# Kernel tuning notes

Hardware: AMD Instinct MI355X
Metric: run time of the kernel (lower is better)

Reference implementation:

```python
import jax, jax.numpy as jnp
import numpy as np

N_NODES = 100000
N_EDGES = 20000  # hyperedges
NNZ = 800000
D = 128


def setup_inputs() -> dict:
    key = jax.random.key(0)
    ks = jax.random.split(key, 10)
    X = jax.random.normal(ks[0], (N_NODES, D), dtype=jnp.float32)
    X0 = jax.random.normal(ks[1], (N_NODES, D), dtype=jnp.float32)
    degE = jax.random.uniform(ks[2], (N_EDGES, 1), dtype=jnp.float32)
    degV = jax.random.uniform(ks[3], (N_NODES, 1), dtype=jnp.float32)
    alpha = jax.random.uniform(ks[4], (1,), dtype=jnp.float32)
    beta = jax.random.uniform(ks[5], (1,), dtype=jnp.float32)
    W_w = jax.random.normal(ks[6], (D, D), dtype=jnp.float32) / np.sqrt(D)
    g1_src = jax.random.randint(ks[7], (NNZ,), 0, N_NODES, dtype=jnp.int64 if jax.config.read('jax_enable_x64') else jnp.int32)
    g1_dst = jax.random.randint(ks[8], (NNZ,), 0, N_EDGES)
    g2_src = jax.random.randint(ks[9], (NNZ,), 0, N_EDGES)
    g2_dst = jax.random.randint(jax.random.fold_in(key, 99), (NNZ,), 0, N_NODES)
    return {"X": X, "X0": X0, "degE": degE, "degV": degV, "alpha": alpha,
            "beta": beta, "W_w": W_w, "g1_src": g1_src, "g1_dst": g1_dst,
            "g2_src": g2_src, "g2_dst": g2_dst}


def reference(X, X0, degE, degV, alpha, beta, W_w, g1_src, g1_dst, g2_src, g2_dst):
    n_edges = degE.shape[0]
    n_nodes = degV.shape[0]
    a = alpha[0]
    b = beta[0]
    # copy_u_sum(g1, X): gather node rows, scatter-sum into hyperedges
    Xe = jax.ops.segment_sum(X[g1_src], g1_dst, num_segments=n_edges)  # [E, D]
    Xe = Xe * degE
    # copy_u_sum(g2, Xe): gather hyperedge rows, scatter-sum into nodes
    Xv = jax.ops.segment_sum(Xe[g2_src], g2_dst, num_segments=n_nodes)  # [N, D]
    Xv = Xv * degV
    # GCNII-style initial residual + identity mapping
    Xi = (1.0 - a) * Xv + a * X0
    out = (1.0 - b) * Xi + b * (Xi @ W_w.T)  # Linear(bias=False)
    return out
```

## Files before the change

kernel.cpp:

```cpp
#include <hip/hip_runtime.h>

#define DD 128
#define SCAN_CHUNK 2048
#define PAD1 16
#define PAD2 8

typedef __attribute__((ext_vector_type(8))) short bf16x8;
typedef __attribute__((ext_vector_type(4))) float f32x4;

__device__ __forceinline__ short f2bf(float f) {
    union { float f; unsigned u; } x; x.f = f;
    unsigned r = x.u + 0x7FFF + ((x.u >> 16) & 1);
    return (short)(r >> 16);
}

__global__ __launch_bounds__(256)
void k_hist2(const int* __restrict__ g1d, const int* __restrict__ g2d,
             int* __restrict__ cnt1p, int* __restrict__ cnt2p,
             int* __restrict__ rank1, int* __restrict__ rank2,
             int nnz, int no) {
    int gid = blockIdx.x * 256 + threadIdx.x;
    const int* dst; int* cnt; int* rank; int q; int str;
    if (gid < no) { dst = g1d; cnt = cnt1p; rank = rank1; str = PAD1; q = gid; }
    else {
        q = gid - no;
        if (q >= no) return;
        dst = g2d; cnt = cnt2p; rank = rank2; str = PAD2;
    }
    int i = q << 3;
    if (i + 8 <= nnz) {
        int4 d0 = *(const int4*)(dst + i);
        int4 d1 = *(const int4*)(dst + i + 4);
        int r0 = atomicAdd(&cnt[d0.x * str], 1);
        int r1 = atomicAdd(&cnt[d0.y * str], 1);
        int r2 = atomicAdd(&cnt[d0.z * str], 1);
        int r3 = atomicAdd(&cnt[d0.w * str], 1);
        int r4 = atomicAdd(&cnt[d1.x * str], 1);
        int r5 = atomicAdd(&cnt[d1.y * str], 1);
        int r6 = atomicAdd(&cnt[d1.z * str], 1);
        int r7 = atomicAdd(&cnt[d1.w * str], 1);
        *(int4*)(rank + i)     = make_int4(r0, r1, r2, r3);
        *(int4*)(rank + i + 4) = make_int4(r4, r5, r6, r7);
    } else {
        for (; i < nnz; ++i) rank[i] = atomicAdd(&cnt[dst[i] * str], 1);
    }
}

__global__ __launch_bounds__(256)
void k_scan_blocks2(const int* __restrict__ cnt1, int* __restrict__ off1,
                    const int* __restrict__ cnt2, int* __restrict__ off2,
                    int* __restrict__ bsum, int n1, int n2, int nb1) {
    __shared__ int sh[256];
    const int tid = threadIdx.x;
    const int b = blockIdx.x;
    const int* cnt; int* off; int* bs; int n; int lb; int str;
    if (b < nb1) { cnt = cnt1; off = off1; bs = bsum;      n = n1; lb = b;       str = PAD1; }
    else         { cnt = cnt2; off = off2; bs = bsum + 64; n = n2; lb = b - nb1; str = PAD2; }

    const int base = lb * SCAN_CHUNK + tid * 8;
    int v[8];
    int s = 0;
    #pragma unroll
    for (int j = 0; j < 8; ++j) {
        int idx = base + j;
        v[j] = (idx < n) ? cnt[(size_t)idx * str] : 0;
        s += v[j];
    }
    sh[tid] = s;
    __syncthreads();
    for (int d = 1; d < 256; d <<= 1) {
        int y = (tid >= d) ? sh[tid - d] : 0;
        __syncthreads();
        sh[tid] += y;
        __syncthreads();
    }
    int incl = sh[tid];
    int run = incl - s;
    #pragma unroll
    for (int j = 0; j < 8; ++j) {
        int idx = base + j;
        if (idx < n) off[idx] = run;
        run += v[j];
    }
    if (tid == 255) bs[lb] = incl;
}

__global__ void k_scan_top2(int* __restrict__ bsum, int nb1, int nb2) {
    if (threadIdx.x == 0) {
        int run = 0;
        for (int i = 0; i < nb1; ++i) { int t = bsum[i]; bsum[i] = run; run += t; }
    } else if (threadIdx.x == 1) {
        int run = 0;
        for (int i = 0; i < nb2; ++i) { int t = bsum[64 + i]; bsum[64 + i] = run; run += t; }
    }
}

__global__ __launch_bounds__(256)
void k_scan_add2(int* __restrict__ off1, int* __restrict__ off2,
                 const int* __restrict__ bsum, int n1, int n2, int nnz) {
    int gid = blockIdx.x * 256 + threadIdx.x;
    if (gid < n1) {
        off1[gid] += bsum[gid >> 11];
    } else {
        int g = gid - n1;
        if (g < n2) off2[g] += bsum[64 + (g >> 11)];
    }
    if (gid == 0) { off1[n1] = nnz; off2[n2] = nnz; }
}

__global__ __launch_bounds__(256)
void k_fill2(const int* __restrict__ g1d, const int* __restrict__ g1s,
             const int* __restrict__ off1, const int* __restrict__ rank1,
             int* __restrict__ srcs1,
             const int* __restrict__ g2d, const int* __restrict__ g2s,
             const int* __restrict__ off2, const int* __restrict__ rank2,
             int* __restrict__ srcs2,
             int nnz, int nq) {
    int gid = blockIdx.x * 256 + threadIdx.x;
    const int* dst; const int* src; const int* off; const int* rank; int* out; int q;
    if (gid < nq) { dst = g1d; src = g1s; off = off1; rank = rank1; out = srcs1; q = gid; }
    else {
        q = gid - nq;
        if (q >= nq) return;
        dst = g2d; src = g2s; off = off2; rank = rank2; out = srcs2;
    }
    int i = q << 2;
    if (i + 4 <= nnz) {
        int4 d = *(const int4*)(dst + i);
        int4 s = *(const int4*)(src + i);
        int4 r = *(const int4*)(rank + i);
        int o0 = off[d.x];
        int o1 = off[d.y];
        int o2 = off[d.z];
        int o3 = off[d.w];
        out[o0 + r.x] = s.x;
        out[o1 + r.y] = s.y;
        out[o2 + r.z] = s.z;
        out[o3 + r.w] = s.w;
    } else {
        for (; i < nnz; ++i) out[off[dst[i]] + rank[i]] = src[i];
    }
}

__global__ __launch_bounds__(256)
void k_edge_gather(const float* __restrict__ X, const int* __restrict__ off,
                   const int* __restrict__ srcs, const float* __restrict__ degE,
                   float* __restrict__ Xe, int n_edges) {
    int gid = blockIdx.x * 256 + threadIdx.x;
    int e = gid >> 5;
    if (e >= n_edges) return;
    int k = (gid & 31) << 2;
    int beg = off[e], end = off[e + 1];
    float4 acc0 = {0, 0, 0, 0}, acc1 = {0, 0, 0, 0};
    float4 acc2 = {0, 0, 0, 0}, acc3 = {0, 0, 0, 0};
    int j = beg;
    for (; j + 8 <= end; j += 8) {
        int s0 = srcs[j + 0];
        int s1 = srcs[j + 1];
        int s2 = srcs[j + 2];
        int s3 = srcs[j + 3];
        int s4 = srcs[j + 4];
        int s5 = srcs[j + 5];
        int s6 = srcs[j + 6];
        int s7 = srcs[j + 7];
        float4 v0 = *(const float4*)(X + (size_t)s0 * DD + k);
        float4 v1 = *(const float4*)(X + (size_t)s1 * DD + k);
        float4 v2 = *(const float4*)(X + (size_t)s2 * DD + k);
        float4 v3 = *(const float4*)(X + (size_t)s3 * DD + k);
        float4 v4 = *(const float4*)(X + (size_t)s4 * DD + k);
        float4 v5 = *(const float4*)(X + (size_t)s5 * DD + k);
        float4 v6 = *(const float4*)(X + (size_t)s6 * DD + k);
        float4 v7 = *(const float4*)(X + (size_t)s7 * DD + k);
        acc0.x += v0.x; acc0.y += v0.y; acc0.z += v0.z; acc0.w += v0.w;
        acc1.x += v1.x; acc1.y += v1.y; acc1.z += v1.z; acc1.w += v1.w;
        acc2.x += v2.x; acc2.y += v2.y; acc2.z += v2.z; acc2.w += v2.w;
        acc3.x += v3.x; acc3.y += v3.y; acc3.z += v3.z; acc3.w += v3.w;
        acc0.x += v4.x; acc0.y += v4.y; acc0.z += v4.z; acc0.w += v4.w;
        acc1.x += v5.x; acc1.y += v5.y; acc1.z += v5.z; acc1.w += v5.w;
        acc2.x += v6.x; acc2.y += v6.y; acc2.z += v6.z; acc2.w += v6.w;
        acc3.x += v7.x; acc3.y += v7.y; acc3.z += v7.z; acc3.w += v7.w;
    }
    for (; j < end; ++j) {
        int s = srcs[j];
        float4 v = *(const float4*)(X + (size_t)s * DD + k);
        acc0.x += v.x; acc0.y += v.y; acc0.z += v.z; acc0.w += v.w;
    }
    float f = degE[e];
    float4 o;
    o.x = f * ((acc0.x + acc1.x) + (acc2.x + acc3.x));
    o.y = f * ((acc0.y + acc1.y) + (acc2.y + acc3.y));
    o.z = f * ((acc0.z + acc1.z) + (acc2.z + acc3.z));
    o.w = f * ((acc0.w + acc1.w) + (acc2.w + acc3.w));
    *(float4*)(Xe + (size_t)e * DD + k) = o;
}

__global__ __launch_bounds__(256)
void k_node_gather(const float* __restrict__ Xe, const int* __restrict__ off,
                   const int* __restrict__ srcs, const float* __restrict__ degV,
                   const float* __restrict__ X0, const float* __restrict__ alphaP,
                   float* __restrict__ Xi, int n_nodes) {
    int gid = blockIdx.x * 256 + threadIdx.x;
    int v = gid >> 5;
    if (v >= n_nodes) return;
    int k = (gid & 31) << 2;
    int beg = off[v], end = off[v + 1];
    float4 acc0 = {0, 0, 0, 0}, acc1 = {0, 0, 0, 0};
    int j = beg;
    for (; j + 4 <= end; j += 4) {
        int s0 = srcs[j + 0];
        int s1 = srcs[j + 1];
        int s2 = srcs[j + 2];
        int s3 = srcs[j + 3];
        float4 v0 = *(const float4*)(Xe + (size_t)s0 * DD + k);
        float4 v1 = *(const float4*)(Xe + (size_t)s1 * DD + k);
        float4 v2 = *(const float4*)(Xe + (size_t)s2 * DD + k);
        float4 v3 = *(const float4*)(Xe + (size_t)s3 * DD + k);
        acc0.x += v0.x; acc0.y += v0.y; acc0.z += v0.z; acc0.w += v0.w;
        acc1.x += v1.x; acc1.y += v1.y; acc1.z += v1.z; acc1.w += v1.w;
        acc0.x += v2.x; acc0.y += v2.y; acc0.z += v2.z; acc0.w += v2.w;
        acc1.x += v3.x; acc1.y += v3.y; acc1.z += v3.z; acc1.w += v3.w;
    }
    for (; j < end; ++j) {
        int s = srcs[j];
        float4 x = *(const float4*)(Xe + (size_t)s * DD + k);
        acc0.x += x.x; acc0.y += x.y; acc0.z += x.z; acc0.w += x.w;
    }
    float a = alphaP[0];
    float f = (1.0f - a) * degV[v];
    float4 x0 = *(const float4*)(X0 + (size_t)v * DD + k);
    float4 o;
    o.x = f * (acc0.x + acc1.x) + a * x0.x;
    o.y = f * (acc0.y + acc1.y) + a * x0.y;
    o.z = f * (acc0.z + acc1.z) + a * x0.z;
    o.w = f * (acc0.w + acc1.w) + a * x0.w;
    *(float4*)(Xi + (size_t)v * DD + k) = o;
}

__global__ __launch_bounds__(256)
void k_prep_w(const float* __restrict__ W, const float* __restrict__ betaP,
              short* __restrict__ Mbf) {
    int gid = blockIdx.x * 256 + threadIdx.x;
    if (gid >= DD * DD / 8) return;
    int c  = gid >> 4;
    int k0 = (gid & 15) << 3;
    float b = betaP[0], ib = 1.0f - b;
    const float* p = W + c * DD + k0;
    float4 lo = *(const float4*)p, hi = *(const float4*)(p + 4);
    float v[8] = {lo.x, lo.y, lo.z, lo.w, hi.x, hi.y, hi.z, hi.w};
    bf16x8 t;
    #pragma unroll
    for (int j = 0; j < 8; ++j) {
        float m = b * v[j] + ((k0 + j) == c ? ib : 0.0f);
        t[j] = f2bf(m);
    }
    *(bf16x8*)(Mbf + (size_t)c * DD + k0) = t;
}

__global__ __launch_bounds__(256)
void k_gemm_mfma(float* xio, const short* __restrict__ Mbf, int n_rows) {
    const int lane = threadIdx.x & 63;
    const int wid  = threadIdx.x >> 6;
    const int m16  = lane & 15;
    const int quad = lane >> 4;
    const int kq   = quad * 8;

    const int strip = blockIdx.x * 4 + wid;
    const int row0 = strip * 16;
    if (row0 >= n_rows) return;

    int arow = row0 + m16;
    if (arow >= n_rows) arow = n_rows - 1;
    const float* xr = xio + (size_t)arow * DD;

    bf16x8 af[4];
    #pragma unroll
    for (int kf = 0; kf < 4; ++kf) {
        const float* p = xr + kf * 32 + kq;
        float4 lo = *(const float4*)p;
        float4 hi = *(const float4*)(p + 4);
        bf16x8 t;
        t[0] = f2bf(lo.x); t[1] = f2bf(lo.y); t[2] = f2bf(lo.z); t[3] = f2bf(lo.w);
        t[4] = f2bf(hi.x); t[5] = f2bf(hi.y); t[6] = f2bf(hi.z); t[7] = f2bf(hi.w);
        af[kf] = t;
    }

    #pragma unroll
    for (int nt = 0; nt < 8; ++nt) {
        const short* mr = Mbf + (size_t)(nt * 16 + m16) * DD + kq;
        f32x4 acc = {0.f, 0.f, 0.f, 0.f};
        #pragma unroll
        for (int kf = 0; kf < 4; ++kf) {
            bf16x8 bfrag = *(const bf16x8*)(mr + kf * 32);
            acc = __builtin_amdgcn_mfma_f32_16x16x32_bf16(af[kf], bfrag, acc, 0, 0, 0);
        }
        const int col = nt * 16 + m16;
        #pragma unroll
        for (int r = 0; r < 4; ++r) {
            int row = row0 + quad * 4 + r;
            if (row < n_rows)
                xio[(size_t)row * DD + col] = acc[r];
        }
    }
}

extern "C" void kernel_launch(void* const* d_in, const int* in_sizes, int n_in,
                              void* d_out, int out_size, void* d_ws, size_t ws_size,
                              hipStream_t stream) {
    const float* X     = (const float*)d_in[0];
    const float* X0    = (const float*)d_in[1];
    const float* degE  = (const float*)d_in[2];
    const float* degV  = (const float*)d_in[3];
    const float* alpha = (const float*)d_in[4];
    const float* beta  = (const float*)d_in[5];
    const float* W     = (const float*)d_in[6];
    const int*   g1s   = (const int*)d_in[7];
    const int*   g1d   = (const int*)d_in[8];
    const int*   g2s   = (const int*)d_in[9];
    const int*   g2d   = (const int*)d_in[10];
    float* out = (float*)d_out;

    const int n_nodes = in_sizes[3];
    const int n_edges = in_sizes[2];
    const int nnz     = in_sizes[7];

    int*   wsi   = (int*)d_ws;
    float* Xe    = (float*)d_ws;
    int*   rank1 = wsi;
    int*   rank2 = wsi + nnz;
    size_t o     = (size_t)n_edges * DD;
    int*   off1  = wsi + o;          o += n_edges + 1;
    int*   off2  = wsi + o;          o += n_nodes + 1;
    size_t srcs_base = o;
    int*   srcs1 = wsi + o;          o += nnz;
    int*   srcs2 = wsi + o;          o += nnz;
    int*   bsum  = wsi + o;          o += 128;
    short* Mbf   = (short*)(wsi + o); o += DD * DD / 2;
    int*   cnt1p = wsi + srcs_base;
    int*   cnt2p = cnt1p + (size_t)n_edges * PAD1;

    hipMemsetAsync(cnt1p, 0,
                   ((size_t)n_edges * PAD1 + (size_t)n_nodes * PAD2) * sizeof(int),
                   stream);

    const int nb1 = (n_edges + SCAN_CHUNK - 1) / SCAN_CHUNK;
    const int nb2 = (n_nodes + SCAN_CHUNK - 1) / SCAN_CHUNK;
    const int no  = (nnz + 7) / 8;
    const int oblb = (2 * no + 255) / 256;
    const int nq  = (nnz + 3) / 4;
    const int qblb = (2 * nq + 255) / 256;

    k_prep_w<<<(DD * DD / 8 + 255) / 256, 256, 0, stream>>>(W, beta, Mbf);

    k_hist2<<<oblb, 256, 0, stream>>>(g1d, g2d, cnt1p, cnt2p, rank1, rank2, nnz, no);
    k_scan_blocks2<<<nb1 + nb2, 256, 0, stream>>>(cnt1p, off1, cnt2p, off2, bsum,
                                                  n_edges, n_nodes, nb1);
    k_scan_top2<<<1, 64, 0, stream>>>(bsum, nb1, nb2);
    k_scan_add2<<<(n_edges + n_nodes + 255) / 256, 256, 0, stream>>>(
        off1, off2, bsum, n_edges, n_nodes, nnz);
    k_fill2<<<qblb, 256, 0, stream>>>(g1d, g1s, off1, rank1, srcs1,
                                      g2d, g2s, off2, rank2, srcs2, nnz, nq);

    k_edge_gather<<<(n_edges * 32 + 255) / 256, 256, 0, stream>>>(
        X, off1, srcs1, degE, Xe, n_edges);
    k_node_gather<<<(n_nodes * 32 + 255) / 256, 256, 0, stream>>>(
        Xe, off2, srcs2, degV, X0, alpha, out, n_nodes);

    const int nstrips = (n_nodes + 15) / 16;
    k_gemm_mfma<<<(nstrips + 3) / 4, 256, 0, stream>>>(out, Mbf, n_nodes);
}
```

Before: 407.6 us.

## Use per-XCD histogram counters with workgroup-scope L2 atomics for CSR build

Replaces the padded, device-scope atomic counters in the histogram pass with eight per-XCD counter arrays. Each CU increments the copy for its own XCC using workgroup-scope atomics, which can resolve in that XCD's L2 rather than needing device-wide coherence. The XCC id is packed into the top bits of each rank. The scan sums the per-XCD counts, scan_add produces a per-XCD base offset table, and the fill step uses tag and base to place entries. This trades cheaper atomics for extra counter reads in the scan, a new base table, and a dependence on workgroup-scope atomics staying coherent within one XCD.

After: 412.9 us. Within noise of the previous version (+1.3%).

```diff
diff --git a/kernel.cpp b/kernel.cpp
--- a/kernel.cpp
+++ b/kernel.cpp
@@ -2,8 +2,7 @@
 
 #define DD 128
 #define SCAN_CHUNK 2048
-#define PAD1 16
-#define PAD2 8
+#define NXCD 8
 
 typedef __attribute__((ext_vector_type(8))) short bf16x8;
 typedef __attribute__((ext_vector_type(4))) float f32x4;
@@ -14,48 +13,63 @@
     return (short)(r >> 16);
 }
 
+__device__ __forceinline__ int xcc_id() {
+    int x;
+    asm volatile("s_getreg_b32 %0, hwreg(HW_REG_XCC_ID)" : "=s"(x));
+    return x & (NXCD - 1);
+}
+
+__device__ __forceinline__ int l2_atomic_inc(int* p) {
+    return __hip_atomic_fetch_add(p, 1, __ATOMIC_RELAXED, __HIP_MEMORY_SCOPE_WORKGROUP);
+}
+
 __global__ __launch_bounds__(256)
 void k_hist2(const int* __restrict__ g1d, const int* __restrict__ g2d,
-             int* __restrict__ cnt1p, int* __restrict__ cnt2p,
+             int* __restrict__ cnt1x, int* __restrict__ cnt2x,
              int* __restrict__ rank1, int* __restrict__ rank2,
-             int nnz, int no) {
+             int nnz, int no, int str1, int str2) {
     int gid = blockIdx.x * 256 + threadIdx.x;
     const int* dst; int* cnt; int* rank; int q; int str;
-    if (gid < no) { dst = g1d; cnt = cnt1p; rank = rank1; str = PAD1; q = gid; }
+    if (gid < no) { dst = g1d; cnt = cnt1x; rank = rank1; str = str1; q = gid; }
     else {
         q = gid - no;
         if (q >= no) return;
-        dst = g2d; cnt = cnt2p; rank = rank2; str = PAD2;
-    }
+        dst = g2d; cnt = cnt2x; rank = rank2; str = str2;
+    }
+    const int xc = xcc_id();
+    int* mycnt = cnt + (size_t)xc * str;
+    const int tag = xc << 24;
+
     int i = q << 3;
     if (i + 8 <= nnz) {
         int4 d0 = *(const int4*)(dst + i);
         int4 d1 = *(const int4*)(dst + i + 4);
-        int r0 = atomicAdd(&cnt[d0.x * str], 1);
-        int r1 = atomicAdd(&cnt[d0.y * str], 1);
-        int r2 = atomicAdd(&cnt[d0.z * str], 1);
-        int r3 = atomicAdd(&cnt[d0.w * str], 1);
-        int r4 = atomicAdd(&cnt[d1.x * str], 1);
-        int r5 = atomicAdd(&cnt[d1.y * str], 1);
-        int r6 = atomicAdd(&cnt[d1.z * str], 1);
-        int r7 = atomicAdd(&cnt[d1.w * str], 1);
-        *(int4*)(rank + i)     = make_int4(r0, r1, r2, r3);
-        *(int4*)(rank + i + 4) = make_int4(r4, r5, r6, r7);
+        int r0 = l2_atomic_inc(&mycnt[d0.x]);
+        int r1 = l2_atomic_inc(&mycnt[d0.y]);
+        int r2 = l2_atomic_inc(&mycnt[d0.z]);
+        int r3 = l2_atomic_inc(&mycnt[d0.w]);
+        int r4 = l2_atomic_inc(&mycnt[d1.x]);
+        int r5 = l2_atomic_inc(&mycnt[d1.y]);
+        int r6 = l2_atomic_inc(&mycnt[d1.z]);
+        int r7 = l2_atomic_inc(&mycnt[d1.w]);
+        *(int4*)(rank + i)     = make_int4(tag | r0, tag | r1, tag | r2, tag | r3);
+        *(int4*)(rank + i + 4) = make_int4(tag | r4, tag | r5, tag | r6, tag | r7);
     } else {
-        for (; i < nnz; ++i) rank[i] = atomicAdd(&cnt[dst[i] * str], 1);
+        for (; i < nnz; ++i) rank[i] = tag | l2_atomic_inc(&mycnt[dst[i]]);
     }
 }
 
 __global__ __launch_bounds__(256)
 void k_scan_blocks2(const int* __restrict__ cnt1, int* __restrict__ off1,
                     const int* __restrict__ cnt2, int* __restrict__ off2,
-                    int* __restrict__ bsum, int n1, int n2, int nb1) {
+                    int* __restrict__ bsum, int n1, int n2, int nb1,
+                    int str1, int str2) {
     __shared__ int sh[256];
     const int tid = threadIdx.x;
     const int b = blockIdx.x;
     const int* cnt; int* off; int* bs; int n; int lb; int str;
-    if (b < nb1) { cnt = cnt1; off = off1; bs = bsum;      n = n1; lb = b;       str = PAD1; }
-    else         { cnt = cnt2; off = off2; bs = bsum + 64; n = n2; lb = b - nb1; str = PAD2; }
+    if (b < nb1) { cnt = cnt1; off = off1; bs = bsum;      n = n1; lb = b;       str = str1; }
+    else         { cnt = cnt2; off = off2; bs = bsum + 64; n = n2; lb = b - nb1; str = str2; }
 
     const int base = lb * SCAN_CHUNK + tid * 8;
     int v[8];
@@ -63,8 +77,13 @@
     #pragma unroll
     for (int j = 0; j < 8; ++j) {
         int idx = base + j;
-        v[j] = (idx < n) ? cnt[(size_t)idx * str] : 0;
-        s += v[j];
+        int t = 0;
+        if (idx < n) {
+            #pragma unroll
+            for (int x = 0; x < NXCD; ++x) t += cnt[(size_t)x * str + idx];
+        }
+        v[j] = t;
+        s += t;
     }
     sh[tid] = s;
     __syncthreads();
@@ -97,48 +116,70 @@
 
 __global__ __launch_bounds__(256)
 void k_scan_add2(int* __restrict__ off1, int* __restrict__ off2,
-                 const int* __restrict__ bsum, int n1, int n2, int nnz) {
+                 const int* __restrict__ bsum,
+                 const int* __restrict__ cnt1x, int* __restrict__ base1,
+                 const int* __restrict__ cnt2x, int* __restrict__ base2,
+                 int n1, int n2, int str1, int str2, int nnz) {
     int gid = blockIdx.x * 256 + threadIdx.x;
     if (gid < n1) {
-        off1[gid] += bsum[gid >> 11];
+        int o = off1[gid] + bsum[gid >> 11];
+        off1[gid] = o;
+        #pragma unroll
+        for (int x = 0; x < NXCD; ++x) {
+            int c = cnt1x[(size_t)x * str1 + gid];
+            base1[(size_t)x * str1 + gid] = o;
+            o += c;
+        }
     } else {
         int g = gid - n1;
-        if (g < n2) off2[g] += bsum[64 + (g >> 11)];
+        if (g < n2) {
+            int o = off2[g] + bsum[64 + (g >> 11)];
+            off2[g] = o;
+            #pragma unroll
+            for (int x = 0; x < NXCD; ++x) {
+                int c = cnt2x[(size_t)x * str2 + g];
+                base2[(size_t)x * str2 + g] = o;
+                o += c;
+            }
+        }
     }
     if (gid == 0) { off1[n1] = nnz; off2[n2] = nnz; }
 }
 
 __global__ __launch_bounds__(256)
 void k_fill2(const int* __restrict__ g1d, const int* __restrict__ g1s,
-             const int* __restrict__ off1, const int* __restrict__ rank1,
+             const int* __restrict__ base1, const int* __restrict__ rank1,
              int* __restrict__ srcs1,
              const int* __restrict__ g2d, const int* __restrict__ g2s,
-             const int* __restrict__ off2, const int* __restrict__ rank2,
+             const int* __restrict__ base2, const int* __restrict__ rank2,
              int* __restrict__ srcs2,
-             int nnz, int nq) {
-    int gid = blockIdx.x * 256 + threadIdx.x;
-    const int* dst; const int* src; const int* off; const int* rank; int* out; int q;
-    if (gid < nq) { dst = g1d; src = g1s; off = off1; rank = rank1; out = srcs1; q = gid; }
+             int nnz, int nq, int str1, int str2) {
+    int gid = blockIdx.x * 256 + threadIdx.x;
+    const int* dst; const int* src; const int* base; const int* rank; int* out; int q; int str;
+    if (gid < nq) { dst = g1d; src = g1s; base = base1; rank = rank1; out = srcs1; str = str1; q = gid; }
     else {
         q = gid - nq;
         if (q >= nq) return;
-        dst = g2d; src = g2s; off = off2; rank = rank2; out = srcs2;
+        dst = g2d; src = g2s; base = base2; rank = rank2; out = srcs2; str = str2;
     }
     int i = q << 2;
     if (i + 4 <= nnz) {
         int4 d = *(const int4*)(dst + i);
         int4 s = *(const int4*)(src + i);
         int4 r = *(const int4*)(rank + i);
-        int o0 = off[d.x];
-        int o1 = off[d.y];
-        int o2 = off[d.z];
-        int o3 = off[d.w];
-        out[o0 + r.x] = s.x;
-        out[o1 + r.y] = s.y;
-        out[o2 + r.z] = s.z;
-        out[o3 + r.w] = s.w;
+        int o0 = base[(size_t)((unsigned)r.x >> 24) * str + d.x] + (r.x & 0xFFFFFF);
+        int o1 = base[(size_t)((unsigned)r.y >> 24) * str + d.y] + (r.y & 0xFFFFFF);
+        int o2 = base[(size_t)((unsigned)r.z >> 24) * str + d.z] + (r.z & 0xFFFFFF);
+        int o3 = base[(size_t)((unsigned)r.w >> 24) * str + d.w] + (r.w & 0xFFFFFF);
+        out[o0] = s.x;
+        out[o1] = s.y;
+        out[o2] = s.z;
+        out[o3] = s.w;
     } else {
-        for (; i < nnz; ++i) out[off[dst[i]] + rank[i]] = src[i];
+        for (; i < nnz; ++i) {
+            int pr = rank[i];
+            out[base[(size_t)((unsigned)pr >> 24) * str + dst[i]] + (pr & 0xFFFFFF)] = src[i];
+        }
     }
 }
 
@@ -323,10 +364,15 @@
     const int n_edges = in_sizes[2];
     const int nnz     = in_sizes[7];
 
+    const int str1 = (n_edges + 15) & ~15;
+    const int str2 = (n_nodes + 15) & ~15;
+
     int*   wsi   = (int*)d_ws;
     float* Xe    = (float*)d_ws;
     int*   rank1 = wsi;
     int*   rank2 = wsi + nnz;
+    int*   base1 = wsi + 2 * (size_t)nnz;
+    int*   base2 = base1 + (size_t)NXCD * str1;
     size_t o     = (size_t)n_edges * DD;
     int*   off1  = wsi + o;          o += n_edges + 1;
     int*   off2  = wsi + o;          o += n_nodes + 1;
@@ -335,12 +381,11 @@
     int*   srcs2 = wsi + o;          o += nnz;
     int*   bsum  = wsi + o;          o += 128;
     short* Mbf   = (short*)(wsi + o); o += DD * DD / 2;
-    int*   cnt1p = wsi + srcs_base;
-    int*   cnt2p = cnt1p + (size_t)n_edges * PAD1;
-
-    hipMemsetAsync(cnt1p, 0,
-                   ((size_t)n_edges * PAD1 + (size_t)n_nodes * PAD2) * sizeof(int),
-                   stream);
+    int*   cnt1x = wsi + srcs_base;
+    int*   cnt2x = cnt1x + (size_t)NXCD * str1;
+
+    hipMemsetAsync(cnt1x, 0,
+                   (size_t)NXCD * (str1 + str2) * sizeof(int), stream);
 
     const int nb1 = (n_edges + SCAN_CHUNK - 1) / SCAN_CHUNK;
     const int nb2 = (n_nodes + SCAN_CHUNK - 1) / SCAN_CHUNK;
@@ -351,14 +396,17 @@
 
     k_prep_w<<<(DD * DD / 8 + 255) / 256, 256, 0, stream>>>(W, beta, Mbf);
 
-    k_hist2<<<oblb, 256, 0, stream>>>(g1d, g2d, cnt1p, cnt2p, rank1, rank2, nnz, no);
-    k_scan_blocks2<<<nb1 + nb2, 256, 0, stream>>>(cnt1p, off1, cnt2p, off2, bsum,
-                                                  n_edges, n_nodes, nb1);
+    k_hist2<<<oblb, 256, 0, stream>>>(g1d, g2d, cnt1x, cnt2x, rank1, rank2,
+                                      nnz, no, str1, str2);
+    k_scan_blocks2<<<nb1 + nb2, 256, 0, stream>>>(cnt1x, off1, cnt2x, off2, bsum,
+                                                  n_edges, n_nodes, nb1, str1, str2);
     k_scan_top2<<<1, 64, 0, stream>>>(bsum, nb1, nb2);
     k_scan_add2<<<(n_edges + n_nodes + 255) / 256, 256, 0, stream>>>(
-        off1, off2, bsum, n_edges, n_nodes, nnz);
-    k_fill2<<<qblb, 256, 0, stream>>>(g1d, g1s, off1, rank1, srcs1,
-                                      g2d, g2s, off2, rank2, srcs2, nnz, nq);
+        off1, off2, bsum, cnt1x, base1, cnt2x, base2,
+        n_edges, n_nodes, str1, str2, nnz);
+    k_fill2<<<qblb, 256, 0, stream>>>(g1d, g1s, base1, rank1, srcs1,
+                                      g2d, g2s, base2, rank2, srcs2,
+                                      nnz, nq, str1, str2);
 
     k_edge_gather<<<(n_edges * 32 + 255) / 256, 256, 0, stream>>>(
         X, off1, srcs1, degE, Xe, n_edges);
```

## Store hyperedge features in bf16 and overlap second histogram with edge gather

Applied to the files above, without the earlier changes.

Stores the intermediate hyperedge features Xe as bf16 instead of fp32. This halves the bytes moved by the random gathers in the node-gather kernel and by the Xe write. The CSR build is split per graph so the g2 histogram runs in the same launch as the edge gather, and the W preparation is folded into the g1 histogram launch. The single-thread top-level scan is replaced by each thread summing preceding block totals. Workspace regions are reused and rank arrays are aliased. Rounding Xe to bf16 adds precision loss to the output.

After: 391.6 us. 3.9% less time.

```diff
diff --git a/kernel.cpp b/kernel.cpp
--- a/kernel.cpp
+++ b/kernel.cpp
@@ -6,6 +6,7 @@
 #define PAD2 8
 
 typedef __attribute__((ext_vector_type(8))) short bf16x8;
+typedef __attribute__((ext_vector_type(4))) short bf16x4;
 typedef __attribute__((ext_vector_type(4))) float f32x4;
 
 __device__ __forceinline__ short f2bf(float f) {
@@ -13,51 +14,62 @@
     unsigned r = x.u + 0x7FFF + ((x.u >> 16) & 1);
     return (short)(r >> 16);
 }
-
-__global__ __launch_bounds__(256)
-void k_hist2(const int* __restrict__ g1d, const int* __restrict__ g2d,
-             int* __restrict__ cnt1p, int* __restrict__ cnt2p,
-             int* __restrict__ rank1, int* __restrict__ rank2,
-             int nnz, int no) {
-    int gid = blockIdx.x * 256 + threadIdx.x;
-    const int* dst; int* cnt; int* rank; int q; int str;
-    if (gid < no) { dst = g1d; cnt = cnt1p; rank = rank1; str = PAD1; q = gid; }
-    else {
-        q = gid - no;
-        if (q >= no) return;
-        dst = g2d; cnt = cnt2p; rank = rank2; str = PAD2;
-    }
+__device__ __forceinline__ float bf2f(short h) {
+    union { float f; unsigned u; } x;
+    x.u = ((unsigned)(unsigned short)h) << 16;
+    return x.f;
+}
+
+__global__ __launch_bounds__(256)
+void k_hist1(const int* __restrict__ g1d, int* __restrict__ cnt1p,
+             int* __restrict__ rank1, int nnz, int no,
+             const float* __restrict__ W, const float* __restrict__ betaP,
+             short* __restrict__ Mbf) {
+    if (blockIdx.x < 8) {
+        int gid = blockIdx.x * 256 + threadIdx.x;
+        if (gid >= DD * DD / 8) return;
+        int c  = gid >> 4;
+        int k0 = (gid & 15) << 3;
+        float b = betaP[0], ib = 1.0f - b;
+        const float* p = W + c * DD + k0;
+        float4 lo = *(const float4*)p, hi = *(const float4*)(p + 4);
+        float v[8] = {lo.x, lo.y, lo.z, lo.w, hi.x, hi.y, hi.z, hi.w};
+        bf16x8 t;
+        #pragma unroll
+        for (int j = 0; j < 8; ++j) {
+            float m = b * v[j] + ((k0 + j) == c ? ib : 0.0f);
+            t[j] = f2bf(m);
+        }
+        *(bf16x8*)(Mbf + (size_t)c * DD + k0) = t;
+        return;
+    }
+    int q = (blockIdx.x - 8) * 256 + threadIdx.x;
+    if (q >= no) return;
     int i = q << 3;
     if (i + 8 <= nnz) {
-        int4 d0 = *(const int4*)(dst + i);
-        int4 d1 = *(const int4*)(dst + i + 4);
-        int r0 = atomicAdd(&cnt[d0.x * str], 1);
-        int r1 = atomicAdd(&cnt[d0.y * str], 1);
-        int r2 = atomicAdd(&cnt[d0.z * str], 1);
-        int r3 = atomicAdd(&cnt[d0.w * str], 1);
-        int r4 = atomicAdd(&cnt[d1.x * str], 1);
-        int r5 = atomicAdd(&cnt[d1.y * str], 1);
-        int r6 = atomicAdd(&cnt[d1.z * str], 1);
-        int r7 = atomicAdd(&cnt[d1.w * str], 1);
-        *(int4*)(rank + i)     = make_int4(r0, r1, r2, r3);
-        *(int4*)(rank + i + 4) = make_int4(r4, r5, r6, r7);
+        int4 d0 = *(const int4*)(g1d + i);
+        int4 d1 = *(const int4*)(g1d + i + 4);
+        int r0 = atomicAdd(&cnt1p[d0.x * PAD1], 1);
+        int r1 = atomicAdd(&cnt1p[d0.y * PAD1], 1);
+        int r2 = atomicAdd(&cnt1p[d0.z * PAD1], 1);
+        int r3 = atomicAdd(&cnt1p[d0.w * PAD1], 1);
+        int r4 = atomicAdd(&cnt1p[d1.x * PAD1], 1);
+        int r5 = atomicAdd(&cnt1p[d1.y * PAD1], 1);
+        int r6 = atomicAdd(&cnt1p[d1.z * PAD1], 1);
+        int r7 = atomicAdd(&cnt1p[d1.w * PAD1], 1);
+        *(int4*)(rank1 + i)     = make_int4(r0, r1, r2, r3);
+        *(int4*)(rank1 + i + 4) = make_int4(r4, r5, r6, r7);
     } else {
-        for (; i < nnz; ++i) rank[i] = atomicAdd(&cnt[dst[i] * str], 1);
-    }
-}
-
-__global__ __launch_bounds__(256)
-void k_scan_blocks2(const int* __restrict__ cnt1, int* __restrict__ off1,
-                    const int* __restrict__ cnt2, int* __restrict__ off2,
-                    int* __restrict__ bsum, int n1, int n2, int nb1) {
+        for (; i < nnz; ++i) rank1[i] = atomicAdd(&cnt1p[g1d[i] * PAD1], 1);
+    }
+}
+
+__global__ __launch_bounds__(256)
+void k_scan_blocks(const int* __restrict__ cnt, int* __restrict__ off,
+                   int* __restrict__ bsum, int n, int str) {
     __shared__ int sh[256];
     const int tid = threadIdx.x;
-    const int b = blockIdx.x;
-    const int* cnt; int* off; int* bs; int n; int lb; int str;
-    if (b < nb1) { cnt = cnt1; off = off1; bs = bsum;      n = n1; lb = b;       str = PAD1; }
-    else         { cnt = cnt2; off = off2; bs = bsum + 64; n = n2; lb = b - nb1; str = PAD2; }
-
-    const int base = lb * SCAN_CHUNK + tid * 8;
+    const int base = blockIdx.x * SCAN_CHUNK + tid * 8;
     int v[8];
     int s = 0;
     #pragma unroll
@@ -82,48 +94,26 @@
         if (idx < n) off[idx] = run;
         run += v[j];
     }
-    if (tid == 255) bs[lb] = incl;
-}
-
-__global__ void k_scan_top2(int* __restrict__ bsum, int nb1, int nb2) {
-    if (threadIdx.x == 0) {
-        int run = 0;
-        for (int i = 0; i < nb1; ++i) { int t = bsum[i]; bsum[i] = run; run += t; }
-    } else if (threadIdx.x == 1) {
-        int run = 0;
-        for (int i = 0; i < nb2; ++i) { int t = bsum[64 + i]; bsum[64 + i] = run; run += t; }
-    }
-}
-
-__global__ __launch_bounds__(256)
-void k_scan_add2(int* __restrict__ off1, int* __restrict__ off2,
-                 const int* __restrict__ bsum, int n1, int n2, int nnz) {
+    if (tid == 255) bsum[blockIdx.x] = incl;
+}
+
+__global__ __launch_bounds__(256)
+void k_scan_add(int* __restrict__ off, const int* __restrict__ bsum,
+                int n, int nnz) {
     int gid = blockIdx.x * 256 + threadIdx.x;
-    if (gid < n1) {
-        off1[gid] += bsum[gid >> 11];
-    } else {
-        int g = gid - n1;
-        if (g < n2) off2[g] += bsum[64 + (g >> 11)];
-    }
-    if (gid == 0) { off1[n1] = nnz; off2[n2] = nnz; }
-}
-
-__global__ __launch_bounds__(256)
-void k_fill2(const int* __restrict__ g1d, const int* __restrict__ g1s,
-             const int* __restrict__ off1, const int* __restrict__ rank1,
-             int* __restrict__ srcs1,
-             const int* __restrict__ g2d, const int* __restrict__ g2s,
-             const int* __restrict__ off2, const int* __restrict__ rank2,
-             int* __restrict__ srcs2,
-             int nnz, int nq) {
-    int gid = blockIdx.x * 256 + threadIdx.x;
-    const int* dst; const int* src; const int* off; const int* rank; int* out; int q;
-    if (gid < nq) { dst = g1d; src = g1s; off = off1; rank = rank1; out = srcs1; q = gid; }
-    else {
-        q = gid - nq;
-        if (q >= nq) return;
-        dst = g2d; src = g2s; off = off2; rank = rank2; out = srcs2;
-    }
+    if (gid == 0) off[n] = nnz;
+    if (gid >= n) return;
+    int chunk = gid >> 11;
+    int p = 0;
+    for (int i = 0; i < chunk; ++i) p += bsum[i];
+    off[gid] += p;
+}
+
+__global__ __launch_bounds__(256)
+void k_fill(const int* __restrict__ dst, const int* __restrict__ src,
+            const int* __restrict__ off, const int* __restrict__ rank,
+            int* __restrict__ out, int nnz, int str) {
+    int q = blockIdx.x * 256 + threadIdx.x;
     int i = q << 2;
     if (i + 4 <= nnz) {
         int4 d = *(const int4*)(dst + i);
@@ -140,29 +130,54 @@
     } else {
         for (; i < nnz; ++i) out[off[dst[i]] + rank[i]] = src[i];
     }
-}
-
-__global__ __launch_bounds__(256)
-void k_edge_gather(const float* __restrict__ X, const int* __restrict__ off,
-                   const int* __restrict__ srcs, const float* __restrict__ degE,
-                   float* __restrict__ Xe, int n_edges) {
-    int gid = blockIdx.x * 256 + threadIdx.x;
+    (void)str;
+}
+
+__global__ __launch_bounds__(256)
+void k_h2_egather(const int* __restrict__ g2d, int* __restrict__ cnt2p,
+                  int* __restrict__ rank2, int nnz, int no, int H,
+                  const float* __restrict__ X, const int* __restrict__ off1,
+                  const int* __restrict__ srcs1, const float* __restrict__ degE,
+                  short* __restrict__ XeBF, int n_edges) {
+    if (blockIdx.x < H) {
+        int q = blockIdx.x * 256 + threadIdx.x;
+        if (q >= no) return;
+        int i = q << 3;
+        if (i + 8 <= nnz) {
+            int4 d0 = *(const int4*)(g2d + i);
+            int4 d1 = *(const int4*)(g2d + i + 4);
+            int r0 = atomicAdd(&cnt2p[d0.x * PAD2], 1);
+            int r1 = atomicAdd(&cnt2p[d0.y * PAD2], 1);
+            int r2 = atomicAdd(&cnt2p[d0.z * PAD2], 1);
+            int r3 = atomicAdd(&cnt2p[d0.w * PAD2], 1);
+            int r4 = atomicAdd(&cnt2p[d1.x * PAD2], 1);
+            int r5 = atomicAdd(&cnt2p[d1.y * PAD2], 1);
+            int r6 = atomicAdd(&cnt2p[d1.z * PAD2], 1);
+            int r7 = atomicAdd(&cnt2p[d1.w * PAD2], 1);
+            *(int4*)(rank2 + i)     = make_int4(r0, r1, r2, r3);
+            *(int4*)(rank2 + i + 4) = make_int4(r4, r5, r6, r7);
+        } else {
+            for (; i < nnz; ++i) rank2[i] = atomicAdd(&cnt2p[g2d[i] * PAD2], 1);
+        }
+        return;
+    }
+    int gid = (blockIdx.x - H) * 256 + threadIdx.x;
     int e = gid >> 5;
     if (e >= n_edges) return;
     int k = (gid & 31) << 2;
-    int beg = off[e], end = off[e + 1];
+    int beg = off1[e], end = off1[e + 1];
     float4 acc0 = {0, 0, 0, 0}, acc1 = {0, 0, 0, 0};
     float4 acc2 = {0, 0, 0, 0}, acc3 = {0, 0, 0, 0};
     int j = beg;
     for (; j + 8 <= end; j += 8) {
-        int s0 = srcs[j + 0];
-        int s1 = srcs[j + 1];
-        int s2 = srcs[j + 2];
-        int s3 = srcs[j + 3];
-        int s4 = srcs[j + 4];
-        int s5 = srcs[j + 5];
-        int s6 = srcs[j + 6];
-        int s7 = srcs[j + 7];
+        int s0 = srcs1[j + 0];
+        int s1 = srcs1[j + 1];
+        int s2 = srcs1[j + 2];
+        int s3 = srcs1[j + 3];
+        int s4 = srcs1[j + 4];
+        int s5 = srcs1[j + 5];
+        int s6 = srcs1[j + 6];
+        int s7 = srcs1[j + 7];
         float4 v0 = *(const float4*)(X + (size_t)s0 * DD + k);
         float4 v1 = *(const float4*)(X + (size_t)s1 * DD + k);
         float4 v2 = *(const float4*)(X + (size_t)s2 * DD + k);
@@ -181,21 +196,21 @@
         acc3.x += v7.x; acc3.y += v7.y; acc3.z += v7.z; acc3.w += v7.w;
     }
     for (; j < end; ++j) {
-        int s = srcs[j];
+        int s = srcs1[j];
         float4 v = *(const float4*)(X + (size_t)s * DD + k);
         acc0.x += v.x; acc0.y += v.y; acc0.z += v.z; acc0.w += v.w;
     }
     float f = degE[e];
-    float4 o;
-    o.x = f * ((acc0.x + acc1.x) + (acc2.x + acc3.x));
-    o.y = f * ((acc0.y + acc1.y) + (acc2.y + acc3.y));
-    o.z = f * ((acc0.z + acc1.z) + (acc2.z + acc3.z));
-    o.w = f * ((acc0.w + acc1.w) + (acc2.w + acc3.w));
-    *(float4*)(Xe + (size_t)e * DD + k) = o;
-}
-
-__global__ __launch_bounds__(256)
-void k_node_gather(const float* __restrict__ Xe, const int* __restrict__ off,
+    bf16x4 ob;
+    ob[0] = f2bf(f * ((acc0.x + acc1.x) + (acc2.x + acc3.x)));
+    ob[1] = f2bf(f * ((acc0.y + acc1.y) + (acc2.y + acc3.y)));
+    ob[2] = f2bf(f * ((acc0.z + acc1.z) + (acc2.z + acc3.z)));
+    ob[3] = f2bf(f * ((acc0.w + acc1.w) + (acc2.w + acc3.w)));
+    *(bf16x4*)(XeBF + (size_t)e * DD + k) = ob;
+}
+
+__global__ __launch_bounds__(256)
+void k_node_gather(const short* __restrict__ XeBF, const int* __restrict__ off,
                    const int* __restrict__ srcs, const float* __restrict__ degV,
                    const float* __restrict__ X0, const float* __restrict__ alphaP,
                    float* __restrict__ Xi, int n_nodes) {
@@ -211,19 +226,19 @@
         int s1 = srcs[j + 1];
         int s2 = srcs[j + 2];
         int s3 = srcs[j + 3];
-        float4 v0 = *(const float4*)(Xe + (size_t)s0 * DD + k);
-        float4 v1 = *(const float4*)(Xe + (size_t)s1 * DD + k);
-        float4 v2 = *(const float4*)(Xe + (size_t)s2 * DD + k);
-        float4 v3 = *(const float4*)(Xe + (size_t)s3 * DD + k);
-        acc0.x += v0.x; acc0.y += v0.y; acc0.z += v0.z; acc0.w += v0.w;
-        acc1.x += v1.x; acc1.y += v1.y; acc1.z += v1.z; acc1.w += v1.w;
-        acc0.x += v2.x; acc0.y += v2.y; acc0.z += v2.z; acc0.w += v2.w;
-        acc1.x += v3.x; acc1.y += v3.y; acc1.z += v3.z; acc1.w += v3.w;
+        bf16x4 h0 = *(const bf16x4*)(XeBF + (size_t)s0 * DD + k);
+        bf16x4 h1 = *(const bf16x4*)(XeBF + (size_t)s1 * DD + k);
+        bf16x4 h2 = *(const bf16x4*)(XeBF + (size_t)s2 * DD + k);
+        bf16x4 h3 = *(const bf16x4*)(XeBF + (size_t)s3 * DD + k);
+        acc0.x += bf2f(h0[0]); acc0.y += bf2f(h0[1]); acc0.z += bf2f(h0[2]); acc0.w += bf2f(h0[3]);
+        acc1.x += bf2f(h1[0]); acc1.y += bf2f(h1[1]); acc1.z += bf2f(h1[2]); acc1.w += bf2f(h1[3]);
+        acc0.x += bf2f(h2[0]); acc0.y += bf2f(h2[1]); acc0.z += bf2f(h2[2]); acc0.w += bf2f(h2[3]);
+        acc1.x += bf2f(h3[0]); acc1.y += bf2f(h3[1]); acc1.z += bf2f(h3[2]); acc1.w += bf2f(h3[3]);
     }
     for (; j < end; ++j) {
         int s = srcs[j];
-        float4 x = *(const float4*)(Xe + (size_t)s * DD + k);
-        acc0.x += x.x; acc0.y += x.y; acc0.z += x.z; acc0.w += x.w;
+        bf16x4 h = *(const bf16x4*)(XeBF + (size_t)s * DD + k);
+        acc0.x += bf2f(h[0]); acc0.y += bf2f(h[1]); acc0.z += bf2f(h[2]); acc0.w += bf2f(h[3]);
     }
     float a = alphaP[0];
     float f = (1.0f - a) * degV[v];
@@ -234,26 +249,6 @@
     o.z = f * (acc0.z + acc1.z) + a * x0.z;
     o.w = f * (acc0.w + acc1.w) + a * x0.w;
     *(float4*)(Xi + (size_t)v * DD + k) = o;
-}
-
-__global__ __launch_bounds__(256)
-void k_prep_w(const float* __restrict__ W, const float* __restrict__ betaP,
-              short* __restrict__ Mbf) {
-    int gid = blockIdx.x * 256 + threadIdx.x;
-    if (gid >= DD * DD / 8) return;
-    int c  = gid >> 4;
-    int k0 = (gid & 15) << 3;
-    float b = betaP[0], ib = 1.0f - b;
-    const float* p = W + c * DD + k0;
-    float4 lo = *(const float4*)p, hi = *(const float4*)(p + 4);
-    float v[8] = {lo.x, lo.y, lo.z, lo.w, hi.x, hi.y, hi.z, hi.w};
-    bf16x8 t;
-    #pragma unroll
-    for (int j = 0; j < 8; ++j) {
-        float m = b * v[j] + ((k0 + j) == c ? ib : 0.0f);
-        t[j] = f2bf(m);
-    }
-    *(bf16x8*)(Mbf + (size_t)c * DD + k0) = t;
 }
 
 __global__ __launch_bounds__(256)
@@ -324,46 +319,45 @@
     const int nnz     = in_sizes[7];
 
     int*   wsi   = (int*)d_ws;
-    float* Xe    = (float*)d_ws;
-    int*   rank1 = wsi;
-    int*   rank2 = wsi + nnz;
-    size_t o     = (size_t)n_edges * DD;
+    short* XeBF  = (short*)d_ws;
+    size_t o     = (size_t)n_edges * DD / 2;
+    int*   rank1 = wsi + o;
+    int*   rank2 = rank1;
+    o += nnz;
     int*   off1  = wsi + o;          o += n_edges + 1;
     int*   off2  = wsi + o;          o += n_nodes + 1;
     size_t srcs_base = o;
     int*   srcs1 = wsi + o;          o += nnz;
     int*   srcs2 = wsi + o;          o += nnz;
-    int*   bsum  = wsi + o;          o += 128;
+    int*   bsum  = wsi + o;          o += 64;
     short* Mbf   = (short*)(wsi + o); o += DD * DD / 2;
     int*   cnt1p = wsi + srcs_base;
-    int*   cnt2p = cnt1p + (size_t)n_edges * PAD1;
-
-    hipMemsetAsync(cnt1p, 0,
-                   ((size_t)n_edges * PAD1 + (size_t)n_nodes * PAD2) * sizeof(int),
-                   stream);
+    int*   cnt2p = wsi + srcs_base + nnz;
+
+    hipMemsetAsync(cnt1p, 0, 2 * (size_t)nnz * sizeof(int), stream);
 
     const int nb1 = (n_edges + SCAN_CHUNK - 1) / SCAN_CHUNK;
     const int nb2 = (n_nodes + SCAN_CHUNK - 1) / SCAN_CHUNK;
     const int no  = (nnz + 7) / 8;
-    const int oblb = (2 * no + 255) / 256;
+    const int hb  = (no + 255) / 256;
     const int nq  = (nnz + 3) / 4;
-    const int qblb = (2 * nq + 255) / 256;
-
-    k_prep_w<<<(DD * DD / 8 + 255) / 256, 256, 0, stream>>>(W, beta, Mbf);
-
-    k_hist2<<<oblb, 256, 0, stream>>>(g1d, g2d, cnt1p, cnt2p, rank1, rank2, nnz, no);
-    k_scan_blocks2<<<nb1 + nb2, 256, 0, stream>>>(cnt1p, off1, cnt2p, off2, bsum,
-                                                  n_edges, n_nodes, nb1);
-    k_scan_top2<<<1, 64, 0, stream>>>(bsum, nb1, nb2);
-    k_scan_add2<<<(n_edges + n_nodes + 255) / 256, 256, 0, stream>>>(
-        off1, off2, bsum, n_edges, n_nodes, nnz);
-    k_fill2<<<qblb, 256, 0, stream>>>(g1d, g1s, off1, rank1, srcs1,
-                                      g2d, g2s, off2, rank2, srcs2, nnz, nq);
-
-    k_edge_gather<<<(n_edges * 32 + 255) / 256, 256, 0, stream>>>(
-        X, off1, srcs1, degE, Xe, n_edges);
+    const int qb  = (nq + 255) / 256;
+
+    k_hist1<<<8 + hb, 256, 0, stream>>>(g1d, cnt1p, rank1, nnz, no, W, beta, Mbf);
+    k_scan_blocks<<<nb1, 256, 0, stream>>>(cnt1p, off1, bsum, n_edges, PAD1);
+    k_scan_add<<<(n_edges + 255) / 256, 256, 0, stream>>>(off1, bsum, n_edges, nnz);
+    k_fill<<<qb, 256, 0, stream>>>(g1d, g1s, off1, rank1, srcs1, nnz, PAD1);
+
+    const int egb = (n_edges * 32 + 255) / 256;
+    k_h2_egather<<<hb + egb, 256, 0, stream>>>(g2d, cnt2p, rank2, nnz, no, hb,
+                                               X, off1, srcs1, degE, XeBF, n_edges);
+
+    k_scan_blocks<<<nb2, 256, 0, stream>>>(cnt2p, off2, bsum, n_nodes, PAD2);
+    k_scan_add<<<(n_nodes + 255) / 256, 256, 0, stream>>>(off2, bsum, n_nodes, nnz);
+    k_fill<<<qb, 256, 0, stream>>>(g2d, g2s, off2, rank2, srcs2, nnz, PAD2);
+
     k_node_gather<<<(n_nodes * 32 + 255) / 256, 256, 0, stream>>>(
-        Xe, off2, srcs2, degV, X0, alpha, out, n_nodes);
+        XeBF, off2, srcs2, degV, X0, alpha, out, n_nodes);
 
     const int nstrips = (n_nodes + 15) / 16;
     k_gemm_mfma<<<(nstrips + 3) / 4, 256, 0, stream>>>(out, Mbf, n_nodes);
```
